# Performance work log

Measured on AMD Instinct MI355X. Metric: run time of the kernel, lower is better.

The kernel has to match this reference:

```python
import jax, jax.numpy as jnp
import numpy as np

N = 50000
E = 800000
IN_CH = 128
HID = 32
HEADS = 4
OUT_CH = 32
NEG_SLOPE = 0.2


def setup_inputs() -> dict:
    key = jax.random.key(0)
    ks = jax.random.split(key, 12)
    x = jax.random.normal(ks[0], (N, IN_CH), dtype=jnp.float32)
    edge_index = jax.random.randint(ks[1], (2, E), 0, N, dtype=jnp.int64)
    s1 = 1.0 / np.sqrt(IN_CH)
    s2 = 1.0 / np.sqrt(HEADS * HID)
    W1 = jax.random.normal(ks[2], (IN_CH, HEADS * HID), dtype=jnp.float32) * s1
    att_src1 = jax.random.normal(ks[3], (HEADS, HID), dtype=jnp.float32) * s2
    att_dst1 = jax.random.normal(ks[4], (HEADS, HID), dtype=jnp.float32) * s2
    b1 = jnp.zeros((HEADS * HID,), dtype=jnp.float32)
    W2 = jax.random.normal(ks[5], (HEADS * HID, OUT_CH), dtype=jnp.float32) * s2
    att_src2 = jax.random.normal(ks[6], (1, OUT_CH), dtype=jnp.float32) * (1.0 / np.sqrt(OUT_CH))
    att_dst2 = jax.random.normal(ks[7], (1, OUT_CH), dtype=jnp.float32) * (1.0 / np.sqrt(OUT_CH))
    b2 = jnp.zeros((OUT_CH,), dtype=jnp.float32)
    return {"x": x, "edge_index": edge_index, "W1": W1, "att_src1": att_src1,
            "att_dst1": att_dst1, "b1": b1, "W2": W2, "att_src2": att_src2,
            "att_dst2": att_dst2, "b2": b2}


def _gat_layer(x, src, dst, W, att_src, att_dst, bias, heads, out_ch, concat):
    n = x.shape[0]
    xw = (x @ W).reshape(n, heads, out_ch)            # [N,H,C]
    a_src = jnp.einsum('nhc,hc->nh', xw, att_src)     # [N,H]
    a_dst = jnp.einsum('nhc,hc->nh', xw, att_dst)
    e = a_src[src] + a_dst[dst]                        # [E,H]
    e = jnp.where(e > 0, e, NEG_SLOPE * e)             # LeakyReLU(0.2)
    # edge-softmax grouped by destination node (stable)
    e_max = jax.ops.segment_max(e, dst, num_segments=n)
    e_max = jnp.where(jnp.isfinite(e_max), e_max, 0.0)
    e_exp = jnp.exp(e - e_max[dst])
    denom = jax.ops.segment_sum(e_exp, dst, num_segments=n)
    alpha = e_exp / (denom[dst] + 1e-16)               # [E,H]
    msg = xw[src] * alpha[:, :, None]                  # [E,H,C]
    out = jax.ops.segment_sum(msg, dst, num_segments=n)  # [N,H,C]
    if concat:
        out = out.reshape(n, heads * out_ch)
    else:
        out = out.mean(axis=1)
    return out + bias


def reference(x, edge_index, W1, att_src1, att_dst1, b1, W2, att_src2, att_dst2, b2):
    # PyG GATConv adds self-loops by default
    loops = jnp.arange(N, dtype=edge_index.dtype)
    src = jnp.concatenate([edge_index[0], loops])
    dst = jnp.concatenate([edge_index[1], loops])
    h = _gat_layer(x, src, dst, W1, att_src1, att_dst1, b1, HEADS, HID, True)
    h = jax.nn.elu(h)
    # dropout p=0.5 is identity at inference (training=False)
    out = _gat_layer(h, src, dst, W2, att_src2, att_dst2, b2, 1, OUT_CH, False)
    return out
```

## Files before the change

### kernel.cpp

```cpp
#include <hip/hip_runtime.h>
#include <hip/hip_fp16.h>

#define N_NODES 50000
#define E_EDGES 800000
#define ETOT (E_EDGES + N_NODES)
#define IN_CH 128
#define HH 128
#define HEADS 4
#define HID 32
#define OUT_CH 32
#define NEG 0.2f

#define GEMM_BLOCKS ((N_NODES + 127) / 128)
#define FILL_BLOCKS ((ETOT + 1023) / 1024)
#define XP 132

__global__ __launch_bounds__(256, 2) void gemm1_fused(const float* __restrict__ x,
                                                      const float* __restrict__ W1,
                                                      const float* __restrict__ att_s,
                                                      const float* __restrict__ att_d,
                                                      const int* __restrict__ ei,
                                                      __half* __restrict__ xwh,
                                                      float* __restrict__ a1s,
                                                      float* __restrict__ a1d,
                                                      int* __restrict__ deg,
                                                      int* __restrict__ idx) {
    __shared__ float Xs[32][XP];
    __shared__ float Ws[32][XP];
    int t = threadIdx.x;

    if (blockIdx.x >= GEMM_BLOCKS) {
        int base = (blockIdx.x - GEMM_BLOCKS) * 1024 + t;
#pragma unroll
        for (int q = 0; q < 4; ++q) {
            int e = base + q * 256;
            if (e < ETOT) {
                int d = (e < E_EDGES) ? ei[E_EDGES + e] : e - E_EDGES;
                idx[e] = atomicAdd(deg + d, 1);
            }
        }
        return;
    }

    int tx = t & 15, ty = t >> 4;
    int row0 = blockIdx.x * 128;
    float acc[8][8] = {};

    for (int k0 = 0; k0 < IN_CH; k0 += 32) {
#pragma unroll
        for (int p = 0; p < 4; ++p) {
            int i2 = t + p * 256;
            int kk = i2 >> 5, c4 = i2 & 31;
            float4 v = *(const float4*)&W1[(size_t)(k0 + kk) * HH + c4 * 4];
            *(float4*)&Ws[kk][c4 * 4] = v;
        }
#pragma unroll
        for (int p = 0; p < 4; ++p) {
            int i2 = t + p * 256;
            int rr = i2 >> 3, c4 = i2 & 7;
            int row = row0 + rr;
            float4 v = make_float4(0.f, 0.f, 0.f, 0.f);
            if (row < N_NODES) v = *(const float4*)&x[(size_t)row * IN_CH + k0 + c4 * 4];
            Xs[c4 * 4 + 0][rr] = v.x;
            Xs[c4 * 4 + 1][rr] = v.y;
            Xs[c4 * 4 + 2][rr] = v.z;
            Xs[c4 * 4 + 3][rr] = v.w;
        }
        __syncthreads();
#pragma unroll 8
        for (int kk = 0; kk < 32; ++kk) {
            float4 xa0 = *(const float4*)&Xs[kk][ty * 4];
            float4 xa1 = *(const float4*)&Xs[kk][ty * 4 + 64];
            float4 wb0 = *(const float4*)&Ws[kk][tx * 4];
            float4 wb1 = *(const float4*)&Ws[kk][tx * 4 + 64];
            float xa[8] = {xa0.x, xa0.y, xa0.z, xa0.w, xa1.x, xa1.y, xa1.z, xa1.w};
            float wb[8] = {wb0.x, wb0.y, wb0.z, wb0.w, wb1.x, wb1.y, wb1.z, wb1.w};
#pragma unroll
            for (int i = 0; i < 8; ++i)
#pragma unroll
                for (int j = 0; j < 8; ++j)
                    acc[i][j] = fmaf(xa[i], wb[j], acc[i][j]);
        }
        __syncthreads();
    }

    float asr[8], adr[8];
#pragma unroll
    for (int j = 0; j < 8; ++j) {
        int col = tx * 4 + (j & 3) + ((j >> 2) << 6);
        asr[j] = att_s[col];
        adr[j] = att_d[col];
    }
    int hA = tx >> 3;

#pragma unroll
    for (int i = 0; i < 8; ++i) {
        int row = row0 + ty * 4 + (i < 4 ? i : 60 + i);
        if (row < N_NODES) {
            union { __half2 h2; unsigned u; } c0, c1, c2, c3;
            c0.h2 = __floats2half2_rn(acc[i][0], acc[i][1]);
            c1.h2 = __floats2half2_rn(acc[i][2], acc[i][3]);
            c2.h2 = __floats2half2_rn(acc[i][4], acc[i][5]);
            c3.h2 = __floats2half2_rn(acc[i][6], acc[i][7]);
            *(uint2*)&xwh[(size_t)row * HH + tx * 4]      = make_uint2(c0.u, c1.u);
            *(uint2*)&xwh[(size_t)row * HH + tx * 4 + 64] = make_uint2(c2.u, c3.u);
        }
        float psA = 0.f, pdA = 0.f, psB = 0.f, pdB = 0.f;
#pragma unroll
        for (int j = 0; j < 4; ++j) {
            psA = fmaf(acc[i][j], asr[j], psA);
            pdA = fmaf(acc[i][j], adr[j], pdA);
            psB = fmaf(acc[i][j + 4], asr[j + 4], psB);
            pdB = fmaf(acc[i][j + 4], adr[j + 4], pdB);
        }
#pragma unroll
        for (int off = 1; off < 8; off <<= 1) {
            psA += __shfl_xor(psA, off, 16);
            pdA += __shfl_xor(pdA, off, 16);
            psB += __shfl_xor(psB, off, 16);
            pdB += __shfl_xor(pdB, off, 16);
        }
        if ((tx & 7) == 0 && row < N_NODES) {
            a1s[row * 4 + hA]     = psA;
            a1d[row * 4 + hA]     = pdA;
            a1s[row * 4 + hA + 2] = psB;
            a1d[row * 4 + hA + 2] = pdB;
        }
    }
}

__device__ __forceinline__ int block_incl_scan(int v, int t) {
    for (int off = 1; off < 64; off <<= 1) {
        int n = __shfl_up(v, off, 64);
        if ((t & 63) >= off) v += n;
    }
    __shared__ int wsum[4];
    if ((t & 63) == 63) wsum[t >> 6] = v;
    __syncthreads();
    int w = t >> 6;
    if (w > 0) {
        int add = 0;
        for (int k = 0; k < w; ++k) add += wsum[k];
        v += add;
    }
    __syncthreads();
    return v;
}

#define NCHUNK ((N_NODES + 255) / 256)

__global__ void scan_s1(const int* __restrict__ deg, int* __restrict__ rowptr,
                        int* __restrict__ partials) {
    int t = threadIdx.x;
    int i = blockIdx.x * 256 + t;
    int v = (i < N_NODES) ? deg[i] : 0;
    int s = block_incl_scan(v, t);
    if (i < N_NODES) rowptr[i + 1] = s;
    if (t == 255) partials[blockIdx.x] = s;
}

__global__ void scan_s2(int* __restrict__ partials) {
    int t = threadIdx.x;
    int v = (t < NCHUNK) ? partials[t] : 0;
    int s = block_incl_scan(v, t);
    if (t < NCHUNK) partials[t] = s;
}

__global__ void scan_s3(int* __restrict__ rowptr, const int* __restrict__ partials) {
    int i = blockIdx.x * blockDim.x + threadIdx.x;
    if (i == 0) rowptr[0] = 0;
    if (i < N_NODES) {
        int c = i >> 8;
        if (c > 0) rowptr[i + 1] += partials[c - 1];
    }
}

__global__ void place_csr(const int* __restrict__ ei, const int* __restrict__ idx,
                          const int* __restrict__ rowptr, int* __restrict__ csr_src) {
    int e = blockIdx.x * blockDim.x + threadIdx.x;
    if (e >= ETOT) return;
    int s, d;
    if (e < E_EDGES) { s = ei[e]; d = ei[E_EDGES + e]; }
    else { s = e - E_EDGES; d = s; }
    csr_src[rowptr[d] + idx[e]] = s;
}

__global__ void gather1(const int* __restrict__ rowptr, const int* __restrict__ csr_src,
                        const float* __restrict__ a1s, const float* __restrict__ a1d,
                        const __half* __restrict__ xwh, float* __restrict__ agg) {
    int t = threadIdx.x;
    int d = blockIdx.x * 4 + (t >> 6);
    if (d >= N_NODES) return;
    int l = t & 63;
    int h = l >> 4;
    float ad = a1d[d * 4 + h];
    int p0 = rowptr[d], p1 = rowptr[d + 1];
    float acc0 = 0.f, acc1 = 0.f, wsum = 0.f;
    int p = p0;
    for (; p + 3 < p1; p += 4) {
        int s0 = csr_src[p], s1 = csr_src[p + 1], s2 = csr_src[p + 2], s3 = csr_src[p + 3];
        float v0 = a1s[s0 * 4 + h] + ad; v0 = v0 > 0.f ? v0 : NEG * v0;
        float v1 = a1s[s1 * 4 + h] + ad; v1 = v1 > 0.f ? v1 : NEG * v1;
        float v2 = a1s[s2 * 4 + h] + ad; v2 = v2 > 0.f ? v2 : NEG * v2;
        float v3 = a1s[s3 * 4 + h] + ad; v3 = v3 > 0.f ? v3 : NEG * v3;
        float w0 = __expf(v0), w1 = __expf(v1), w2 = __expf(v2), w3 = __expf(v3);
        float2 f0 = __half22float2(*(const __half2*)&xwh[(size_t)s0 * HH + 2 * l]);
        float2 f1 = __half22float2(*(const __half2*)&xwh[(size_t)s1 * HH + 2 * l]);
        float2 f2 = __half22float2(*(const __half2*)&xwh[(size_t)s2 * HH + 2 * l]);
        float2 f3 = __half22float2(*(const __half2*)&xwh[(size_t)s3 * HH + 2 * l]);
        acc0 = fmaf(w0, f0.x, acc0); acc1 = fmaf(w0, f0.y, acc1);
        acc0 = fmaf(w1, f1.x, acc0); acc1 = fmaf(w1, f1.y, acc1);
        acc0 = fmaf(w2, f2.x, acc0); acc1 = fmaf(w2, f2.y, acc1);
        acc0 = fmaf(w3, f3.x, acc0); acc1 = fmaf(w3, f3.y, acc1);
        wsum += (w0 + w1) + (w2 + w3);
    }
    for (; p < p1; ++p) {
        int s = csr_src[p];
        float v = a1s[s * 4 + h] + ad; v = v > 0.f ? v : NEG * v;
        float w = __expf(v);
        float2 f = __half22float2(*(const __half2*)&xwh[(size_t)s * HH + 2 * l]);
        acc0 = fmaf(w, f.x, acc0); acc1 = fmaf(w, f.y, acc1);
        wsum += w;
    }
    float r = 1.f / (wsum + 1e-16f);
    *(float2*)&agg[(size_t)d * HH + 2 * l] = make_float2(acc0 * r, acc1 * r);
}

__global__ void gemm2_kernel(const float* __restrict__ agg1,
                             const float* __restrict__ b1,
                             const float* __restrict__ W2,
                             const float* __restrict__ att_s,
                             const float* __restrict__ att_d,
                             __half* __restrict__ hw2h,
                             float* __restrict__ a2s,
                             float* __restrict__ a2d) {
    __shared__ float Wl[HH * OUT_CH];
    __shared__ float hs[8][HH];
    int t = threadIdx.x;
    for (int i = t; i < HH * OUT_CH; i += 256) Wl[i] = W2[i];
    __syncthreads();
    int nChunks = (N_NODES + 7) / 8;
    for (int ch = blockIdx.x; ch < nChunks; ch += gridDim.x) {
        int row0 = ch * 8;
        __syncthreads();
        for (int i = t; i < 8 * HH; i += 256) {
            int rr = i >> 7, jj = i & 127;
            int row = row0 + rr;
            if (row < N_NODES) {
                float v = agg1[(size_t)row * HH + jj] + b1[jj];
                hs[rr][jj] = v > 0.f ? v : (__expf(v) - 1.f);
            }
        }
        __syncthreads();
        int r = t >> 5, o = t & 31;
        int row = row0 + r;
        if (row < N_NODES) {
            float acc = 0.f;
#pragma unroll 4
            for (int jj = 0; jj < HH; ++jj) acc = fmaf(hs[r][jj], Wl[jj * OUT_CH + o], acc);
            hw2h[(size_t)row * OUT_CH + o] = __float2half_rn(acc);
            float ps = acc * att_s[o], pd = acc * att_d[o];
            for (int off = 16; off; off >>= 1) {
                ps += __shfl_down(ps, off, 32);
                pd += __shfl_down(pd, off, 32);
            }
            if (o == 0) { a2s[row] = ps; a2d[row] = pd; }
        }
    }
}

__global__ void gather2(const int* __restrict__ rowptr, const int* __restrict__ csr_src,
                        const float* __restrict__ a2s, const float* __restrict__ a2d,
                        const __half* __restrict__ hw2h, const float* __restrict__ b2,
                        float* __restrict__ out) {
    int t = threadIdx.x;
    int d = blockIdx.x * 8 + (t >> 5);
    if (d >= N_NODES) return;
    int o = t & 31;
    float ad = a2d[d];
    int p0 = rowptr[d], p1 = rowptr[d + 1];
    float acc = 0.f, wsum = 0.f;
    int p = p0;
    for (; p + 3 < p1; p += 4) {
        int s0 = csr_src[p], s1 = csr_src[p + 1], s2 = csr_src[p + 2], s3 = csr_src[p + 3];
        float v0 = a2s[s0] + ad; v0 = v0 > 0.f ? v0 : NEG * v0;
        float v1 = a2s[s1] + ad; v1 = v1 > 0.f ? v1 : NEG * v1;
        float v2 = a2s[s2] + ad; v2 = v2 > 0.f ? v2 : NEG * v2;
        float v3 = a2s[s3] + ad; v3 = v3 > 0.f ? v3 : NEG * v3;
        float w0 = __expf(v0), w1 = __expf(v1), w2 = __expf(v2), w3 = __expf(v3);
        float x0 = __half2float(hw2h[(size_t)s0 * OUT_CH + o]);
        float x1 = __half2float(hw2h[(size_t)s1 * OUT_CH + o]);
        float x2 = __half2float(hw2h[(size_t)s2 * OUT_CH + o]);
        float x3 = __half2float(hw2h[(size_t)s3 * OUT_CH + o]);
        acc = fmaf(w0, x0, acc); acc = fmaf(w1, x1, acc);
        acc = fmaf(w2, x2, acc); acc = fmaf(w3, x3, acc);
        wsum += (w0 + w1) + (w2 + w3);
    }
    for (; p < p1; ++p) {
        int s = csr_src[p];
        float v = a2s[s] + ad; v = v > 0.f ? v : NEG * v;
        float w = __expf(v);
        acc = fmaf(w, __half2float(hw2h[(size_t)s * OUT_CH + o]), acc);
        wsum += w;
    }
    out[(size_t)d * OUT_CH + o] = acc / (wsum + 1e-16f) + b2[o];
}

extern "C" void kernel_launch(void* const* d_in, const int* in_sizes, int n_in,
                              void* d_out, int out_size, void* d_ws, size_t ws_size,
                              hipStream_t stream) {
    const float* x   = (const float*)d_in[0];
    const int*   ei  = (const int*)d_in[1];
    const float* W1  = (const float*)d_in[2];
    const float* as1 = (const float*)d_in[3];
    const float* ad1 = (const float*)d_in[4];
    const float* b1  = (const float*)d_in[5];
    const float* W2  = (const float*)d_in[6];
    const float* as2 = (const float*)d_in[7];
    const float* ad2 = (const float*)d_in[8];
    const float* b2  = (const float*)d_in[9];
    float* out = (float*)d_out;
    float* ws  = (float*)d_ws;

    __half* xwh   = (__half*)ws;
    __half* hw2h  = (__half*)ws;
    float* agg1   = ws + 3200000;
    float* a1s    = ws + 9600000;
    float* a1d    = ws + 9800000;
    float* a2s    = a1s;
    float* a2d    = a1d;
    int*   deg    = (int*)(ws + 10000000);
    int*   rowptr = (int*)(ws + 10050000);
    int*   parts  = (int*)(ws + 10100016);
    int*   csr_src= (int*)(ws + 10100272);
    int*   idx    = (int*)(ws + 10950272);

    hipMemsetAsync(deg, 0, (size_t)N_NODES * sizeof(int), stream);

    gemm1_fused<<<GEMM_BLOCKS + FILL_BLOCKS, 256, 0, stream>>>(
        x, W1, as1, ad1, ei, xwh, a1s, a1d, deg, idx);

    scan_s1  <<<NCHUNK, 256, 0, stream>>>(deg, rowptr, parts);
    scan_s2  <<<1, 256, 0, stream>>>(parts);
    scan_s3  <<<(N_NODES + 255) / 256, 256, 0, stream>>>(rowptr, parts);
    place_csr<<<(ETOT + 255) / 256, 256, 0, stream>>>(ei, idx, rowptr, csr_src);

    gather1  <<<(N_NODES + 3) / 4, 256, 0, stream>>>(rowptr, csr_src, a1s, a1d, xwh, agg1);

    gemm2_kernel<<<2048, 256, 0, stream>>>(agg1, b1, W2, as2, ad2, hw2h, a2s, a2d);
    gather2  <<<(N_NODES + 7) / 8, 256, 0, stream>>>(rowptr, csr_src, a2s, a2d, hw2h, b2, out);
}
```

Baseline: 178.1 us.

## Fuse layer-1 aggregation with layer-2 projection into one kernel

The layer-1 neighbour aggregation kernel now applies bias and ELU itself and immediately multiplies each node's row by W2 from shared memory. It then writes the half-precision projected features and the layer-2 attention scores directly. This removes the fp32 agg1 intermediate's write and read-back, plus one kernel launch. In exchange, every 4-node block reloads the full 16KB W2 into LDS, which adds a lot of L2 traffic and limits occupancy. The in-wave shared-memory handoff also relies on 64-wide wavefront execution with no barrier.

Measured after the change: 172.8 us. 3.0% less time.

```diff
diff --git a/kernel.cpp b/kernel.cpp
--- a/kernel.cpp
+++ b/kernel.cpp
@@ -185,12 +185,21 @@
     csr_src[rowptr[d] + idx[e]] = s;
 }
 
-__global__ void gather1(const int* __restrict__ rowptr, const int* __restrict__ csr_src,
-                        const float* __restrict__ a1s, const float* __restrict__ a1d,
-                        const __half* __restrict__ xwh, float* __restrict__ agg) {
-    int t = threadIdx.x;
-    int d = blockIdx.x * 4 + (t >> 6);
-    if (d >= N_NODES) return;
+__global__ void gather1_g2(const int* __restrict__ rowptr, const int* __restrict__ csr_src,
+                           const float* __restrict__ a1s, const float* __restrict__ a1d,
+                           const __half* __restrict__ xwh,
+                           const float* __restrict__ b1, const float* __restrict__ W2,
+                           const float* __restrict__ att_s2, const float* __restrict__ att_d2,
+                           __half* __restrict__ hw2h,
+                           float* __restrict__ a2s, float* __restrict__ a2d) {
+    __shared__ float Wl[HH * OUT_CH];
+    __shared__ float hs[4][HH];
+    int t = threadIdx.x;
+    for (int i = t; i < HH * OUT_CH; i += 256) Wl[i] = W2[i];
+    __syncthreads();
+
+    int wid = t >> 6;
+    int d = blockIdx.x * 4 + wid;
     int l = t & 63;
     int h = l >> 4;
     float ad = a1d[d * 4 + h];
@@ -223,50 +232,30 @@
         wsum += w;
     }
     float r = 1.f / (wsum + 1e-16f);
-    *(float2*)&agg[(size_t)d * HH + 2 * l] = make_float2(acc0 * r, acc1 * r);
-}
-
-__global__ void gemm2_kernel(const float* __restrict__ agg1,
-                             const float* __restrict__ b1,
-                             const float* __restrict__ W2,
-                             const float* __restrict__ att_s,
-                             const float* __restrict__ att_d,
-                             __half* __restrict__ hw2h,
-                             float* __restrict__ a2s,
-                             float* __restrict__ a2d) {
-    __shared__ float Wl[HH * OUT_CH];
-    __shared__ float hs[8][HH];
-    int t = threadIdx.x;
-    for (int i = t; i < HH * OUT_CH; i += 256) Wl[i] = W2[i];
-    __syncthreads();
-    int nChunks = (N_NODES + 7) / 8;
-    for (int ch = blockIdx.x; ch < nChunks; ch += gridDim.x) {
-        int row0 = ch * 8;
-        __syncthreads();
-        for (int i = t; i < 8 * HH; i += 256) {
-            int rr = i >> 7, jj = i & 127;
-            int row = row0 + rr;
-            if (row < N_NODES) {
-                float v = agg1[(size_t)row * HH + jj] + b1[jj];
-                hs[rr][jj] = v > 0.f ? v : (__expf(v) - 1.f);
-            }
-        }
-        __syncthreads();
-        int r = t >> 5, o = t & 31;
-        int row = row0 + r;
-        if (row < N_NODES) {
-            float acc = 0.f;
-#pragma unroll 4
-            for (int jj = 0; jj < HH; ++jj) acc = fmaf(hs[r][jj], Wl[jj * OUT_CH + o], acc);
-            hw2h[(size_t)row * OUT_CH + o] = __float2half_rn(acc);
-            float ps = acc * att_s[o], pd = acc * att_d[o];
-            for (int off = 16; off; off >>= 1) {
-                ps += __shfl_down(ps, off, 32);
-                pd += __shfl_down(pd, off, 32);
-            }
-            if (o == 0) { a2s[row] = ps; a2d[row] = pd; }
-        }
-    }
+    float2 bv = *(const float2*)&b1[2 * l];
+    float h0 = acc0 * r + bv.x;
+    float h1 = acc1 * r + bv.y;
+    h0 = h0 > 0.f ? h0 : (__expf(h0) - 1.f);
+    h1 = h1 > 0.f ? h1 : (__expf(h1) - 1.f);
+    *(float2*)&hs[wid][2 * l] = make_float2(h0, h1);
+
+    int o = l & 31, half = l >> 5;
+    const float* hrow = &hs[wid][half * 64];
+    const float* wcol = &Wl[half * 64 * OUT_CH + o];
+    float acc = 0.f;
+#pragma unroll 8
+    for (int j = 0; j < 64; ++j) acc = fmaf(hrow[j], wcol[j * OUT_CH], acc);
+    acc += __shfl_xor(acc, 32, 64);
+
+    if (half == 0) hw2h[(size_t)d * OUT_CH + o] = __float2half_rn(acc);
+
+    float ps = acc * att_s2[o], pd = acc * att_d2[o];
+#pragma unroll
+    for (int off = 16; off; off >>= 1) {
+        ps += __shfl_xor(ps, off, 32);
+        pd += __shfl_xor(pd, off, 32);
+    }
+    if (l == 0) { a2s[d] = ps; a2d[d] = pd; }
 }
 
 __global__ void gather2(const int* __restrict__ rowptr, const int* __restrict__ csr_src,
@@ -323,17 +312,16 @@
     float* ws  = (float*)d_ws;
 
     __half* xwh   = (__half*)ws;
-    __half* hw2h  = (__half*)ws;
-    float* agg1   = ws + 3200000;
-    float* a1s    = ws + 9600000;
-    float* a1d    = ws + 9800000;
-    float* a2s    = a1s;
-    float* a2d    = a1d;
-    int*   deg    = (int*)(ws + 10000000);
-    int*   rowptr = (int*)(ws + 10050000);
-    int*   parts  = (int*)(ws + 10100016);
-    int*   csr_src= (int*)(ws + 10100272);
-    int*   idx    = (int*)(ws + 10950272);
+    __half* hw2h  = (__half*)(ws + 3200000);
+    float* a1s    = ws + 4000000;
+    float* a1d    = ws + 4200000;
+    float* a2s    = ws + 4400000;
+    float* a2d    = ws + 4450000;
+    int*   deg    = (int*)(ws + 4500000);
+    int*   rowptr = (int*)(ws + 4550000);
+    int*   parts  = (int*)(ws + 4600016);
+    int*   csr_src= (int*)(ws + 4600272);
+    int*   idx    = (int*)(ws + 5450272);
 
     hipMemsetAsync(deg, 0, (size_t)N_NODES * sizeof(int), stream);
 
@@ -345,8 +333,8 @@
     scan_s3  <<<(N_NODES + 255) / 256, 256, 0, stream>>>(rowptr, parts);
     place_csr<<<(ETOT + 255) / 256, 256, 0, stream>>>(ei, idx, rowptr, csr_src);
 
-    gather1  <<<(N_NODES + 3) / 4, 256, 0, stream>>>(rowptr, csr_src, a1s, a1d, xwh, agg1);
-
-    gemm2_kernel<<<2048, 256, 0, stream>>>(agg1, b1, W2, as2, ad2, hw2h, a2s, a2d);
+    gather1_g2<<<N_NODES / 4, 256, 0, stream>>>(rowptr, csr_src, a1s, a1d, xwh,
+                                                b1, W2, as2, ad2, hw2h, a2s, a2d);
+
     gather2  <<<(N_NODES + 7) / 8, 256, 0, stream>>>(rowptr, csr_src, a2s, a2d, hw2h, b2, out);
 }
```
